# Kernel optimization log

Hardware: AMD Instinct MI355X
Metric: run time of the kernel (lower is better)

Reference implementation:

```python
import jax, jax.numpy as jnp
import numpy as np

EPS = 1e-6
NEG = 0.2  # leaky-relu negative slope
OBJ_C = 6

def _knn(x, k):
    # x: [B,3,N] -> [B,N,k] indices of k nearest neighbors (incl. self)
    xx = jnp.sum(x * x, axis=1)
    inner = jnp.einsum('bdn,bdm->bnm', x, x)
    pd = 2.0 * inner - xx[:, :, None] - xx[:, None, :]  # negative sq dist
    return jax.lax.top_k(pd, k)[1]

def _gather_pts(xt, idx):
    # xt [B,N,D], idx [B,N,k] -> [B,N,k,D]
    return xt[jnp.arange(xt.shape[0])[:, None, None], idx]

def _vn_lin(W, x):
    # channel-mixing linear over VN channel dim: x [B,Cin,3,...]
    return jnp.einsum('oc,bc...->bo...', W, x)

def _vn_bn(x, g, b, eps=1e-5):
    # VNBatchNorm with batch statistics on vector norms
    n = jnp.linalg.norm(x, axis=2) + EPS          # [B,C,*spatial]
    axes = (0,) + tuple(range(2, n.ndim))
    m = jnp.mean(n, axes, keepdims=True)
    v = jnp.var(n, axes, keepdims=True)
    shp = (1, -1) + (1,) * (n.ndim - 2)
    nb = g.reshape(shp) * (n - m) / jnp.sqrt(v + eps) + b.reshape(shp)
    return x / n[:, :, None] * nb[:, :, None]

def _vn_leaky(p, d):
    dot = jnp.sum(p * d, axis=2, keepdims=True)
    dsq = jnp.sum(d * d, axis=2, keepdims=True)
    return NEG * p + (1.0 - NEG) * jnp.where(dot >= 0, p, p - (dot / (dsq + EPS)) * d)

def _vn_block(x, wf, wd, g=None, b=None):
    # VNLinearLeakyReLU
    p = _vn_lin(wf, x)
    if g is not None:
        p = _vn_bn(p, g, b)
    return _vn_leaky(p, _vn_lin(wd, x))

def _surface_feature(coord, k):
    # coord [B,3,N] -> [B,3(chan),3(vec),N,k]: (nb-ctr, ctr, nb x ctr)
    idx = _knn(coord, k)
    xt = coord.transpose(0, 2, 1)                                  # [B,N,3]
    nb = _gather_pts(xt, idx)[:, :, :, None, :]                    # [B,N,k,1,3]
    ctr = jnp.broadcast_to(xt[:, :, None, None, :], nb.shape)
    f = jnp.concatenate([nb - ctr, ctr, jnp.cross(nb, ctr, axis=-1)], axis=3)
    return f.transpose(0, 3, 4, 1, 2)

def _neighbor_feature(x, coord, k):
    # x [B,C,3,N], knn over coord -> [B,C,3,N,k]
    B, C, _, N = x.shape
    idx = _knn(coord, k)
    xt = x.reshape(B, C * 3, N).transpose(0, 2, 1)                 # [B,N,C*3]
    f = _gather_pts(xt, idx).reshape(B, N, k, C, 3)
    return f.transpose(0, 3, 4, 1, 2)

def _vn_maxpool_down(x, coord, wd, rate):
    # x [B,C,3,N,k]: stride-subsample points, VN-max over k neighbors
    x = x[:, :, :, ::rate, :]
    coord_d = coord[:, :, ::rate]
    dot = jnp.sum(x * _vn_lin(wd, x), axis=2)                      # [B,C,Nd,k]
    idx = jnp.argmax(dot, axis=-1)
    xm = jnp.take_along_axis(x, idx[:, :, None, :, None], axis=-1)[..., 0]
    return xm, coord_d

def _nearest_index(t, s):
    # t [B,N,3], s [B,M,3] -> argmin sq-dist index [B,N]
    d = jnp.sum(t * t, -1)[:, :, None] - 2.0 * jnp.einsum('bnd,bmd->bnm', t, s) + jnp.sum(s * s, -1)[:, None, :]
    return jnp.argmin(d, axis=-1)

def _index_points(x, idx):
    # x [B,C,3,M], idx [B,N] -> [B,C,3,N]
    xt = x.transpose(0, 3, 1, 2)
    return xt[jnp.arange(x.shape[0])[:, None], idx].transpose(0, 2, 3, 1)

def _conv_bn_relu(x, w, b, g, be, eps=1e-5):
    # 1x1 Conv1d + BatchNorm1d (batch stats) + ReLU
    y = jnp.einsum('oc,bcn->bon', w, x) + b[None, :, None]
    m = jnp.mean(y, (0, 2), keepdims=True)
    v = jnp.var(y, (0, 2), keepdims=True)
    return jax.nn.relu(g[None, :, None] * (y - m) / jnp.sqrt(v + eps) + be[None, :, None])

def _forward(x, norm, cat_id, wf0, wd0, g0, b0, wf1, wd1, g1, b1, wp1, wf2, wd2, g2, b2, wf3, wd3, g3, b3, wp2, wf4, wd4, g4, b4, wv1f, wv1d, wv2f, wv2d, w3, ws1, cb1, sg1, sb1, ws2, cb2, sg2, sb2, ws3, cb3, sg3, sb3):
    B, _, _, N = x.shape
    coord = x.reshape(B, 3, N)
    one_hot = jax.nn.one_hot(cat_id, OBJ_C, dtype=x.dtype)
    x0 = _vn_block(_surface_feature(coord, 20), wf0, wd0, g0, b0).mean(-1)   # [B,42,3,N]
    x1 = _vn_block(x0, wf1, wd1, g1, b1)
    x2, coord2 = _vn_maxpool_down(_neighbor_feature(x1, coord, 4), coord, wp1, 4)
    x2 = _vn_block(x2, wf2, wd2, g2, b2)                                     # [B,84,3,N/4]
    x3 = _vn_block(x2, wf3, wd3, g3, b3)
    x4, coord4 = _vn_maxpool_down(_neighbor_feature(x3, coord2, 4), coord2, wp2, 4)
    x4 = _vn_block(x4, wf4, wd4, g4, b4)                                     # [B,168,3,N/16]
    ct = coord.transpose(0, 2, 1)
    i1 = _nearest_index(ct, coord2.transpose(0, 2, 1))
    i2 = _nearest_index(ct, coord4.transpose(0, 2, 1))
    eqv = jnp.concatenate([x0, x1, _index_points(x2, i1), _index_points(x3, i1), _index_points(x4, i2)], axis=1)  # [B,420,3,N]
    mean_feat = eqv.mean(-1, keepdims=True)                                  # [B,420,3,1]
    z = _vn_block(mean_feat, wv1f, wv1d)
    z = _vn_block(z, wv2f, wv2d)
    z = jnp.einsum('bcvm,kc->bvkm', z, w3)                                   # [B,3,2,1]
    inv_gl = jnp.einsum('bijm,bjkm->bikm', mean_feat, z).reshape(B, -1, 1)   # [B,840,1]
    inv_0 = jnp.broadcast_to(inv_gl, (B, inv_gl.shape[1], N))
    inv_1 = jnp.sum(mean_feat * coord[:, None], axis=2)                      # [B,420,N]
    oh = jnp.broadcast_to(one_hot[:, :, None], (B, OBJ_C, N))
    inv = jnp.concatenate([norm, inv_0, inv_1, oh], axis=1)                  # [B,1267,N]
    inv = _conv_bn_relu(inv, ws1, cb1, sg1, sb1)
    inv = _conv_bn_relu(inv, ws2, cb2, sg2, sb2)
    inv = _conv_bn_relu(inv, ws3, cb3, sg3, sb3)                             # [B,420,N]
    return eqv, mean_feat, inv, inv_gl

def setup_inputs():
    key = jax.random.key(0)
    ki = iter(jax.random.split(key, 40))
    B, N, D = 4, 2048, 42
    def lin(o, c):
        return jax.random.normal(next(ki), (o, c), jnp.float32) / float(np.sqrt(c))
    inp = dict(
        x=jax.random.normal(next(ki), (B, 1, 3, N), jnp.float32),
        norm=jax.random.normal(next(ki), (B, 1, N), jnp.float32),
        cat_id=jax.random.randint(next(ki), (B,), 0, OBJ_C),
        wf0=lin(D, 3), wd0=lin(D, 3), g0=jnp.ones(D), b0=jnp.zeros(D),
        wf1=lin(D, D), wd1=lin(D, D), g1=jnp.ones(D), b1=jnp.zeros(D),
        wp1=lin(D, D),
        wf2=lin(2 * D, D), wd2=lin(2 * D, D), g2=jnp.ones(2 * D), b2=jnp.zeros(2 * D),
        wf3=lin(2 * D, 2 * D), wd3=lin(2 * D, 2 * D), g3=jnp.ones(2 * D), b3=jnp.zeros(2 * D),
        wp2=lin(2 * D, 2 * D),
        wf4=lin(4 * D, 2 * D), wd4=lin(4 * D, 2 * D), g4=jnp.ones(4 * D), b4=jnp.zeros(4 * D),
        wv1f=lin(5 * D, 10 * D), wv1d=lin(5 * D, 10 * D),
        wv2f=lin(2 * D, 5 * D), wv2d=lin(2 * D, 5 * D),
        w3=lin(2, 2 * D),
        ws1=lin(1024, 1267), cb1=jnp.zeros(1024), sg1=jnp.ones(1024), sb1=jnp.zeros(1024),
        ws2=lin(512, 1024), cb2=jnp.zeros(512), sg2=jnp.ones(512), sb2=jnp.zeros(512),
        ws3=lin(420, 512), cb3=jnp.zeros(420), sg3=jnp.ones(420), sb3=jnp.zeros(420),
    )
    return inp

def reference(x, norm, cat_id, wf0, wd0, g0, b0, wf1, wd1, g1, b1, wp1, wf2, wd2, g2, b2, wf3, wd3, g3, b3, wp2, wf4, wd4, g4, b4, wv1f, wv1d, wv2f, wv2d, w3, ws1, cb1, sg1, sb1, ws2, cb2, sg2, sb2, ws3, cb3, sg3, sb3):
    return _forward(x, norm, cat_id, wf0, wd0, g0, b0, wf1, wd1, g1, b1, wp1, wf2, wd2, g2, b2, wf3, wd3, g3, b3, wp2, wf4, wd4, g4, b4, wv1f, wv1d, wv2f, wv2d, w3, ws1, cb1, sg1, sb1, ws2, cb2, sg2, sb2, ws3, cb3, sg3, sb3)
```

## Files before the change

kernel.cpp:

```cpp
#include <hip/hip_runtime.h>
#include <hip/hip_bf16.h>
#include <cstdint>
#include <cstddef>

#define NTOT 2048
#define BTOT 4

typedef short bf16x8 __attribute__((ext_vector_type(8)));
typedef float f32x4 __attribute__((ext_vector_type(4)));

__device__ inline unsigned short f2b(float v) {
    __hip_bfloat16 h = __float2bfloat16(v);
    return *reinterpret_cast<unsigned short*>(&h);
}

static const size_t WS_IDX20 = 0;
static const size_t WS_X1T   = 163840;
static const size_t WS_X0    = 1638400;
static const size_t WS_X1    = 3702784;
static const size_t WS_XM2   = 5767168;
static const size_t WS_X2    = 6025216;
static const size_t WS_X3    = 6541312;
static const size_t WS_IDX42 = 7057408;
static const size_t WS_XM4   = 7059456;
static const size_t WS_X4    = 7188480;
static const size_t WS_I1    = 7446528;
static const size_t WS_I2    = 7454720;
static const size_t WS_MF    = 7462912;
static const size_t WS_INVGL = 7467952;
static const size_t WS_STATS = 7471312;
static const size_t WS_CST   = 7472992;
static const size_t WS_CB    = 7480320;
static const size_t WS_AB    = 7484416;
static const size_t WS_W0    = 7496704;
static const size_t WS_Z1    = 7497728;
static const size_t WS_Z2    = 7500288;
static const size_t WS_X3T   = 7501312;
static const size_t WS_W2B   = 13378560;
static const size_t WS_W3B   = 13640704;
static const size_t WS_Y1B   = 0;
static const size_t WS_Y2T   = 7480320;
static const size_t WS_Y2B   = 4194304;
static const size_t WS_Y3T   = 13771776;

#define ZERO_SPAN_BYTES ((7476904 - 7462912) * 4)

#define ST0_OFF 0
#define ST1_OFF 84
#define ST2_OFF 168
#define ST3_OFF 336
#define ST4_OFF 504
#define CST1_OFF 0
#define CST2_OFF 2048
#define CST3_OFF 3072

#define OUT_EQV   0
#define OUT_MF    10321920
#define OUT_INV   10326960
#define OUT_INVGL 13767600

template <int SLOTS, int K, int NQ>
__global__ __launch_bounds__(256)
void knn_reg_kernel(const float* __restrict__ coord, int cand_stride, int q_stride,
                    int* __restrict__ out_idx, int q_cnt)
{
#pragma clang fp contract(off)
    constexpr int Q = SLOTS / 8;
    int b = blockIdx.y;
    int wave = threadIdx.x >> 6, lane = threadIdx.x & 63;
// ... 170 lines not shown
            float cx = ctr[ps * 3], cy = ctr[ps * 3 + 1], cz = ctr[ps * 3 + 2];
            const float* nb = &nbc[ps * 60];
            float sf = 0.f, sf2 = 0.f;
            for (int k = 0; k < 20; ++k) {
                float nx = nb[k * 3], ny = nb[k * 3 + 1], nz = nb[k * 3 + 2];
                float dx = nx - cx, dy = ny - cy, dz = nz - cz;
                float crx = ny * cz - nz * cy;
                float cry = nz * cx - nx * cz;
                float crz = nx * cy - ny * cx;
                float p0 = w0 * dx + w1 * cx + w2 * crx;
                float p1 = w0 * dy + w1 * cy + w2 * cry;
                float p2 = w0 * dz + w1 * cz + w2 * crz;
                float nrm = sqrtf(p0 * p0 + p1 * p1 + p2 * p2) + 1e-6f;
                sf += nrm; sf2 += nrm * nrm;
            }
            s += (double)sf; s2 += (double)sf2;
        }
    }
    if (active) { red[0][ps][o] = s; red[1][ps][o] = s2; }
    __syncthreads();
    if (t < 42) {
        double a = 0.0, a2 = 0.0;
#pragma unroll
        for (int p = 0; p < 6; ++p) { a += red[0][p][t]; a2 += red[1][p][t]; }
        atomicAdd(&stats[t], a);
        atomicAdd(&stats[42 + t], a2);
    }
}

__global__ __launch_bounds__(256)
void apply0_kernel(const float* __restrict__ coord, const int* __restrict__ idx20,
                   const float* __restrict__ wf0, const float* __restrict__ wd0,
                   const float* __restrict__ g0, const float* __restrict__ b0,
                   const double* __restrict__ stats, float* __restrict__ x0)
{
    __shared__ float nbc[360];
    __shared__ float ctr[18];
    int t = threadIdx.x;
    int b = blockIdx.y;
    int ps = t / 42, o = t - ps * 42;
    int n0 = blockIdx.x * 6;
    if (t < 120) {
        int pl = t / 20, k = t - pl * 20;
        int n = n0 + pl; if (n > NTOT - 1) n = NTOT - 1;
        int m = idx20[((size_t)(b * NTOT + n)) * 20 + k];
        nbc[t * 3 + 0] = coord[(b * 3 + 0) * NTOT + m];
        nbc[t * 3 + 1] = coord[(b * 3 + 1) * NTOT + m];
        nbc[t * 3 + 2] = coord[(b * 3 + 2) * NTOT + m];
    }
    if (t >= 128 && t < 146) {
        int i = t - 128; int pl = i / 3, vd = i - pl * 3;
        int n = n0 + pl; if (n > NTOT - 1) n = NTOT - 1;
        ctr[i] = coord[(b * 3 + vd) * NTOT + n];
    }
    __syncthreads();
    int n = n0 + ps;
    if (ps >= 6 || n >= NTOT) return;
    double S1 = stats[o], S2 = stats[42 + o];
    double md = S1 / 163840.0;
    float m = (float)md;
    float var = (float)(S2 / 163840.0 - md * md);
    float gs = g0[o] / sqrtf(var + 1e-5f);
    float bb = b0[o];
    float wa0 = wf0[o * 3], wa1 = wf0[o * 3 + 1], wa2 = wf0[o * 3 + 2];
    float wb0 = wd0[o * 3], wb1 = wd0[o * 3 + 1], wb2 = wd0[o * 3 + 2];
    float cx = ctr[ps * 3], cy = ctr[ps * 3 + 1], cz = ctr[ps * 3 + 2];
    const float* nb = &nbc[ps * 60];
    float a0 = 0.f, a1 = 0.f, a2 = 0.f;
    for (int k = 0; k < 20; ++k) {
        float nx = nb[k * 3], ny = nb[k * 3 + 1], nz = nb[k * 3 + 2];
        float dx = nx - cx, dy = ny - cy, dz = nz - cz;
        float crx = ny * cz - nz * cy;
        float cry = nz * cx - nx * cz;
        float crz = nx * cy - ny * cx;
        float p0 = wa0 * dx + wa1 * cx + wa2 * crx;
        float p1 = wa0 * dy + wa1 * cy + wa2 * cry;
        float p2 = wa0 * dz + wa1 * cz + wa2 * crz;
        float d0 = wb0 * dx + wb1 * cx + wb2 * crx;
        float d1 = wb0 * dy + wb1 * cy + wb2 * cry;
        float d2 = wb0 * dz + wb1 * cz + wb2 * crz;
        float nrm = sqrtf(p0 * p0 + p1 * p1 + p2 * p2) + 1e-6f;
        float nbv = gs * (nrm - m) + bb;
        float sc = nbv / nrm;
        p0 *= sc; p1 *= sc; p2 *= sc;
        float dot = p0 * d0 + p1 * d1 + p2 * d2;
        float dsq = d0 * d0 + d1 * d1 + d2 * d2 + 1e-6f;
        float tq = fminf(dot, 0.f) / dsq;
        a0 += 0.2f * p0 + 0.8f * (p0 - tq * d0);
        a1 += 0.2f * p1 + 0.8f * (p1 - tq * d1);
        a2 += 0.2f * p2 + 0.8f * (p2 - tq * d2);
    }
    x0[((size_t)(b * 42 + o) * 3 + 0) * NTOT + n] = a0 / 20.0f;
    x0[((size_t)(b * 42 + o) * 3 + 1) * NTOT + n] = a1 / 20.0f;
    x0[((size_t)(b * 42 + o) * 3 + 2) * NTOT + n] = a2 / 20.0f;
}

template <int Ci, int Co, int PTS, int NT, int NIT>
__global__ __launch_bounds__(NT)
void vn_stats_kernel(const float* __restrict__ xin,
                     const float* __restrict__ wf,
                     double* __restrict__ stats, int Npts)
{
    constexpr int Ci3 = Ci * 3;
    constexpr int STRIDE = Ci3 + 1;
    __shared__ float col[PTS * STRIDE];
    __shared__ double red[2][PTS][Co];
    int t = threadIdx.x;
    int b = blockIdx.y;
    int ps = t / Co;
    int o = t - ps * Co;
    bool active = ps < PTS;
    double s = 0.0, s2 = 0.0;
    int base = blockIdx.x * (PTS * NIT);
    for (int it = 0; it < NIT; ++it) {
        int pt0 = base + it * PTS;
        __syncthreads();
        for (int i = t; i < PTS * Ci3; i += NT) {
            int pl = i / Ci3, off = i - pl * Ci3;
            int pt = pt0 + pl; if (pt >= Npts) pt = Npts - 1;
            col[pl * STRIDE + off] = xin[(size_t)(b * 3 * Ci + off) * Npts + pt];
        }
        __syncthreads();
        if (active && pt0 + ps < Npts) {
            const float* cl = &col[ps * STRIDE];
            const float* wr = wf + o * Ci;
            float p0 = 0.f, p1 = 0.f, p2 = 0.f;
#pragma unroll
            for (int c = 0; c < Ci; ++c) {
                float w = wr[c];
                p0 += w * cl[3 * c]; p1 += w * cl[3 * c + 1]; p2 += w * cl[3 * c + 2];
            }
            float nrm = sqrtf(p0 * p0 + p1 * p1 + p2 * p2) + 1e-6f;
            s += (double)nrm; s2 += (double)nrm * (double)nrm;
        }
    }
    if (active) { red[0][ps][o] = s; red[1][ps][o] = s2; }
    __syncthreads();
    if (t < Co) {
        double a = 0.0, a2 = 0.0;
#pragma unroll
        for (int p = 0; p < PTS; ++p) { a += red[0][p][t]; a2 += red[1][p][t]; }
        atomicAdd(&stats[t], a);
        atomicAdd(&stats[Co + t], a2);
    }
}

template <int Ci, int Co, int PTS, int NT, bool WT>
__global__ __launch_bounds__(NT)
void vn_apply_kernel(const float* __restrict__ xin,
                     const float* __restrict__ wf,
                     const float* __restrict__ wd,
                     const float* __restrict__ g,
                     const float* __restrict__ bbp,
                     const double* __restrict__ stats,
                     double count, int Npts,
                     float* __restrict__ xout,
                     float* __restrict__ xt)
{
    constexpr int Ci3 = Ci * 3;
    constexpr int STRIDE = Ci3 + 1;
    constexpr int CH = Co * 3;
    __shared__ float col[PTS * STRIDE];
    int t = threadIdx.x;
    int b = blockIdx.y;
    int ps = t / Co;
    int o = t - ps * Co;
    bool active = ps < PTS;
    float m = 0.f, gs = 0.f, bb = 0.f;
    if (active) {
        double S1 = stats[o], S2 = stats[Co + o];
        double md = S1 / count;
        m = (float)md;
        float var = (float)(S2 / count - md * md);
        gs = g[o] / sqrtf(var + 1e-5f);
        bb = bbp[o];
    }
    int pt0 = blockIdx.x * PTS;
    for (int i = t; i < PTS * Ci3; i += NT) {
        int pl = i / Ci3, off = i - pl * Ci3;
        int pt = pt0 + pl; if (pt >= Npts) pt = Npts - 1;
        col[pl * STRIDE + off] = xin[(size_t)(b * 3 * Ci + off) * Npts + pt];
    }
    __syncthreads();
    int pt = pt0 + ps;
    if (!active || pt >= Npts) return;
    const float* cl = &col[ps * STRIDE];
    const float* wr = wf + o * Ci;
    const float* wdr = wd + o * Ci;
    float p0 = 0.f, p1 = 0.f, p2 = 0.f, d0 = 0.f, d1 = 0.f, d2 = 0.f;
#pragma unroll
    for (int c = 0; c < Ci; ++c) {
        float c0 = cl[3 * c], c1 = cl[3 * c + 1], c2 = cl[3 * c + 2];
        float w = wr[c];
        p0 += w * c0; p1 += w * c1; p2 += w * c2;
        float w2 = wdr[c];
        d0 += w2 * c0; d1 += w2 * c1; d2 += w2 * c2;
    }
    float nrm = sqrtf(p0 * p0 + p1 * p1 + p2 * p2) + 1e-6f;
    float nb = gs * (nrm - m) + bb;
    float sc = nb / nrm;
    p0 *= sc; p1 *= sc; p2 *= sc;
    float dot = p0 * d0 + p1 * d1 + p2 * d2;
    float dsq = d0 * d0 + d1 * d1 + d2 * d2 + 1e-6f;
    float tq = fminf(dot, 0.f) / dsq;
    float r0 = p0 - tq * d0, r1 = p1 - tq * d1, r2 = p2 - tq * d2;
    float o0 = 0.2f * p0 + 0.8f * r0;
    float o1 = 0.2f * p1 + 0.8f * r1;
    float o2 = 0.2f * p2 + 0.8f * r2;
    xout[((size_t)(b * Co + o) * 3 + 0) * Npts + pt] = o0;
    xout[((size_t)(b * Co + o) * 3 + 1) * Npts + pt] = o1;
    xout[((size_t)(b * Co + o) * 3 + 2) * Npts + pt] = o2;
    if (WT) {
        float* tp = xt + ((size_t)(b * Npts + pt)) * CH + o * 3;
        tp[0] = o0; tp[1] = o1; tp[2] = o2;
    }
}

__global__ void vn_pool_kernel(const float* __restrict__ xint,
                               const int* __restrict__ idx, long long sb, int sq,
                               const float* __restrict__ wp,
                               float* __restrict__ xout,
                               int C, int Np, int Nq)
{
#pragma clang fp contract(off)
    __shared__ float nb[4 * 84 * 3];
    int b = blockIdx.y;
    int q = blockIdx.x;
    const int* ir = idx + b * sb + (long long)q * sq;
    int CH = C * 3;
    for (int kk = 0; kk < 4; ++kk) {
        int mm = ir[kk];
        const float* src = xint + ((size_t)(b * Np + mm)) * CH;
        for (int t = threadIdx.x; t < CH; t += blockDim.x)
            nb[kk * CH + t] = src[t];
    }
    __syncthreads();
    int o = threadIdx.x;
    if (o >= C) return;
    const float* wr = wp + o * C;
    float best = -3.4e38f;
    int bk = 0;
    for (int kk = 0; kk < 4; ++kk) {
        const float* cl = &nb[kk * CH];
        float d0 = 0.f, d1 = 0.f, d2 = 0.f;
        for (int c = 0; c < C; ++c) {
            float w = wr[c];
            d0 += w * cl[3 * c]; d1 += w * cl[3 * c + 1]; d2 += w * cl[3 * c + 2];
// ... 12 lines not shown
                           const float* __restrict__ x4,
                           const int* __restrict__ i1, const int* __restrict__ i2,
                           float* __restrict__ out_eqv, float* __restrict__ mfw)
{
    __shared__ float wsum[4];
    int n = blockIdx.x * 256 + threadIdx.x;
    int cv = blockIdx.y;
    int b = blockIdx.z;
    int cc = cv / 3, v = cv % 3;
    float val;
    if (cc < 42)
        val = x0[((size_t)(b * 42 + cc) * 3 + v) * NTOT + n];
    else if (cc < 84)
        val = x1[((size_t)(b * 42 + (cc - 42)) * 3 + v) * NTOT + n];
    else if (cc < 168) {
        int m = i1[b * NTOT + n];
        val = x2[((size_t)(b * 84 + (cc - 84)) * 3 + v) * 512 + m];
    } else if (cc < 252) {
        int m = i1[b * NTOT + n];
        val = x3[((size_t)(b * 84 + (cc - 168)) * 3 + v) * 512 + m];
    } else {
        int m = i2[b * NTOT + n];
        val = x4[((size_t)(b * 168 + (cc - 252)) * 3 + v) * 128 + m];
    }
    out_eqv[((size_t)(b * 1260 + cv)) * NTOT + n] = val;
    float s = val;
    for (int off = 32; off; off >>= 1) s += __shfl_down(s, off);
    if ((threadIdx.x & 63) == 0) wsum[threadIdx.x >> 6] = s;
    __syncthreads();
    if (threadIdx.x == 0)
        atomicAdd(&mfw[b * 1260 + cv], (wsum[0] + wsum[1]) + (wsum[2] + wsum[3]));
}

__global__ void mf_finalize_kernel(float* __restrict__ mfw, float* __restrict__ out_mf)
{
    int i = blockIdx.x * 256 + threadIdx.x;
    if (i < 5040) {
        float m = mfw[i] / 2048.0f;
        mfw[i] = m;
        out_mf[i] = m;
    }
}

__global__ __launch_bounds__(256)
void z1_kernel(const float* __restrict__ mfw,
               const float* __restrict__ wv1f, const float* __restrict__ wv1d,
               float* __restrict__ z1ws)
{
    __shared__ float mf[1260];
    int b = blockIdx.y;
    int wave = threadIdx.x >> 6, lane = threadIdx.x & 63;
    for (int i = threadIdx.x; i < 1260; i += 256) mf[i] = mfw[b * 1260 + i];
    __syncthreads();
    int o = blockIdx.x * 4 + wave;
    if (o >= 210) return;
    const float* wr  = wv1f + (size_t)o * 420;
    const float* wdr = wv1d + (size_t)o * 420;
    float p0 = 0.f, p1 = 0.f, p2 = 0.f, d0 = 0.f, d1 = 0.f, d2 = 0.f;
    for (int c = lane; c < 420; c += 64) {
        float m0 = mf[3 * c], m1 = mf[3 * c + 1], m2 = mf[3 * c + 2];
        float w = wr[c];
        p0 += w * m0; p1 += w * m1; p2 += w * m2;
        float w2 = wdr[c];
        d0 += w2 * m0; d1 += w2 * m1; d2 += w2 * m2;
    }
    for (int off = 32; off; off >>= 1) {
        p0 += __shfl_down(p0, off); p1 += __shfl_down(p1, off);
        p2 += __shfl_down(p2, off); d0 += __shfl_down(d0, off);
        d1 += __shfl_down(d1, off); d2 += __shfl_down(d2, off);
    }
    if (lane == 0) {
        float dot = p0 * d0 + p1 * d1 + p2 * d2;
        float r0, r1, r2;
        if (dot >= 0.f) { r0 = p0; r1 = p1; r2 = p2; }
        else {
            float tq = dot / (d0 * d0 + d1 * d1 + d2 * d2 + 1e-6f);
            r0 = p0 - tq * d0; r1 = p1 - tq * d1; r2 = p2 - tq * d2;
        }
        z1ws[b * 630 + o * 3]     = 0.2f * p0 + 0.8f * r0;
        z1ws[b * 630 + o * 3 + 1] = 0.2f * p1 + 0.8f * r1;
        z1ws[b * 630 + o * 3 + 2] = 0.2f * p2 + 0.8f * r2;
    }
}

__global__ __launch_bounds__(256)
void z2_kernel(const float* __restrict__ z1ws,
               const float* __restrict__ wv2f, const float* __restrict__ wv2d,
               float* __restrict__ z2ws)
{
    __shared__ float zl[630];
    int b = blockIdx.y;
    int wave = threadIdx.x >> 6, lane = threadIdx.x & 63;
    for (int i = threadIdx.x; i < 630; i += 256) zl[i] = z1ws[b * 630 + i];
    __syncthreads();
    int o = blockIdx.x * 4 + wave;
    if (o >= 84) return;
    const float* wr  = wv2f + (size_t)o * 210;
    const float* wdr = wv2d + (size_t)o * 210;
    float p0 = 0.f, p1 = 0.f, p2 = 0.f, d0 = 0.f, d1 = 0.f, d2 = 0.f;
    for (int c = lane; c < 210; c += 64) {
        float m0 = zl[3 * c], m1 = zl[3 * c + 1], m2 = zl[3 * c + 2];
        float w = wr[c];
        p0 += w * m0; p1 += w * m1; p2 += w * m2;
        float w2 = wdr[c];
        d0 += w2 * m0; d1 += w2 * m1; d2 += w2 * m2;
    }
    for (int off = 32; off; off >>= 1) {
        p0 += __shfl_down(p0, off); p1 += __shfl_down(p1, off);
        p2 += __shfl_down(p2, off); d0 += __shfl_down(d0, off);
        d1 += __shfl_down(d1, off); d2 += __shfl_down(d2, off);
    }
    if (lane == 0) {
        float dot = p0 * d0 + p1 * d1 + p2 * d2;
        float r0, r1, r2;
        if (dot >= 0.f) { r0 = p0; r1 = p1; r2 = p2; }
        else {
            float tq = dot / (d0 * d0 + d1 * d1 + d2 * d2 + 1e-6f);
            r0 = p0 - tq * d0; r1 = p1 - tq * d1; r2 = p2 - tq * d2;
        }
        z2ws[b * 252 + o * 3]     = 0.2f * p0 + 0.8f * r0;
        z2ws[b * 252 + o * 3 + 1] = 0.2f * p1 + 0.8f * r1;
        z2ws[b * 252 + o * 3 + 2] = 0.2f * p2 + 0.8f * r2;
    }
}

__global__ void z3invgl_kernel(const float* __restrict__ mfw,
                               const float* __restrict__ z2ws,
                               const float* __restrict__ w3,
                               float* __restrict__ invgl_ws,
                               float* __restrict__ out_invgl)
{
    __shared__ float z2[252];
    __shared__ float z3[6];
    __shared__ float mf[1260];
    int b = blockIdx.x;
    int t = threadIdx.x;
    for (int i = t; i < 252; i += 256) z2[i] = z2ws[b * 252 + i];
    for (int i = t; i < 1260; i += 256) mf[i] = mfw[b * 1260 + i];
    __syncthreads();
    if (t < 6) {
        int v = t / 2, kt = t % 2;
        float s = 0.f;
        for (int c = 0; c < 84; ++c) s += z2[c * 3 + v] * w3[kt * 84 + c];
        z3[v * 2 + kt] = s;
    }
    __syncthreads();
    for (int i = t; i < 840; i += 256) {
        int ii = i / 2, kt = i % 2;
        float s = mf[ii * 3] * z3[0 + kt] + mf[ii * 3 + 1] * z3[2 + kt] +
                  mf[ii * 3 + 2] * z3[4 + kt];
        invgl_ws[b * 840 + i] = s;
        out_invgl[b * 840 + i] = s;
    }
}

__global__ __launch_bounds__(256)
void conv1_coef_kernel(const float* __restrict__ ws1,
                       const float* __restrict__ invgl,
                       const float* __restrict__ mfw,
                       const int* __restrict__ cat,
                       float* __restrict__ cb, float* __restrict__ ab,
                       float* __restrict__ w0)
{
    int wave = threadIdx.x >> 6, lane = threadIdx.x & 63;
    int o = blockIdx.x * 4 + wave;
    int b = blockIdx.y;
    const float* wr = ws1 + (size_t)o * 1267;
    float s = 0.f;
    for (int j = lane; j < 840; j += 64)
        s += wr[1 + j] * invgl[b * 840 + j];
    float a0 = 0.f, a1 = 0.f, a2 = 0.f;
    for (int i = lane; i < 420; i += 64) {
        float w = wr[841 + i];
        a0 += w * mfw[b * 1260 + i * 3];
        a1 += w * mfw[b * 1260 + i * 3 + 1];
        a2 += w * mfw[b * 1260 + i * 3 + 2];
    }
    for (int off = 32; off; off >>= 1) {
        s  += __shfl_down(s, off);
        a0 += __shfl_down(a0, off);
        a1 += __shfl_down(a1, off);
        a2 += __shfl_down(a2, off);
    }
// ... 248 lines not shown
    const float* w3   = (const float*)d_in[29];
    const float* ws1  = (const float*)d_in[30];
    const float* sg1  = (const float*)d_in[32];
    const float* sb1  = (const float*)d_in[33];
    const float* ws2  = (const float*)d_in[34];
    const float* sg2  = (const float*)d_in[36];
    const float* sb2  = (const float*)d_in[37];
    const float* ws3  = (const float*)d_in[38];
    const float* sg3  = (const float*)d_in[40];
    const float* sb3  = (const float*)d_in[41];

    float* ws = (float*)d_ws;
    float* out = (float*)d_out;

    int*    idx20 = (int*)(ws + WS_IDX20);
    float*  x1t   = ws + WS_X1T;
    float*  x0    = ws + WS_X0;
    float*  x1    = ws + WS_X1;
    float*  xm2   = ws + WS_XM2;
    float*  x2    = ws + WS_X2;
    float*  x3    = ws + WS_X3;
    int*    idx42 = (int*)(ws + WS_IDX42);
    float*  xm4   = ws + WS_XM4;
    float*  x4    = ws + WS_X4;
    int*    i1p   = (int*)(ws + WS_I1);
    int*    i2p   = (int*)(ws + WS_I2);
    float*  mfw   = ws + WS_MF;
    float*  invgl = ws + WS_INVGL;
    double* st    = (double*)(ws + WS_STATS);
    float*  cst   = ws + WS_CST;
    float*  cb    = ws + WS_CB;
    float*  ab    = ws + WS_AB;
    float*  w0    = ws + WS_W0;
    float*  z1ws  = ws + WS_Z1;
    float*  z2ws  = ws + WS_Z2;
    float*  x3t   = ws + WS_X3T;
    unsigned short* w2b  = (unsigned short*)(ws + WS_W2B);
    unsigned short* w3b  = (unsigned short*)(ws + WS_W3B);
    unsigned short* y1b  = (unsigned short*)(ws + WS_Y1B);
    float*  y2t   = ws + WS_Y2T;
    unsigned short* y2b  = (unsigned short*)(ws + WS_Y2B);
    float*  y3t   = ws + WS_Y3T;

    hipMemsetAsync((void*)mfw, 0, ZERO_SPAN_BYTES, stream);

    wconv_kernel<<<dim3(4, 512), 256, 0, stream>>>(ws2, w2b, 512, 1024, 1024);
    wconv_kernel<<<dim3(2, 512), 256, 0, stream>>>(ws3, w3b, 420, 512, 512);

    knn_reg_kernel<32, 20, 2><<<dim3(256, 4), 256, 0, stream>>>(xc, 1, 1, idx20, 2048);

    stats0_kernel<<<dim3(43, 4), 256, 0, stream>>>(xc, idx20, wf0, st + ST0_OFF);
    apply0_kernel<<<dim3(342, 4), 256, 0, stream>>>(xc, idx20, wf0, wd0, g0, b0,
                                                    st + ST0_OFF, x0);

    vn_stats_kernel<42, 42, 6, 256, 8><<<dim3(43, 4), 256, 0, stream>>>(
        x0, wf1, st + ST1_OFF, 2048);
    vn_apply_kernel<42, 42, 6, 256, true><<<dim3(342, 4), 256, 0, stream>>>(
        x0, wf1, wd1, g1, b1, st + ST1_OFF, 8192.0, 2048, x1, x1t);

    vn_pool_kernel<<<dim3(512, 4), 256, 0, stream>>>(x1t, idx20, 40960LL, 80, wp1, xm2,
                                                     42, 2048, 512);
    vn_stats_kernel<42, 84, 3, 256, 8><<<dim3(22, 4), 256, 0, stream>>>(
        xm2, wf2, st + ST2_OFF, 512);
    vn_apply_kernel<42, 84, 3, 256, false><<<dim3(171, 4), 256, 0, stream>>>(
        xm2, wf2, wd2, g2, b2, st + ST2_OFF, 2048.0, 512, x2, nullptr);
    vn_stats_kernel<84, 84, 3, 256, 8><<<dim3(22, 4), 256, 0, stream>>>(
        x2, wf3, st + ST3_OFF, 512);
    vn_apply_kernel<84, 84, 3, 256, true><<<dim3(171, 4), 256, 0, stream>>>(
        x2, wf3, wd3, g3, b3, st + ST3_OFF, 2048.0, 512, x3, x3t);

    knn_reg_kernel<8, 4, 1><<<dim3(32, 4), 256, 0, stream>>>(xc, 4, 16, idx42, 128);
    vn_pool_kernel<<<dim3(128, 4), 256, 0, stream>>>(x3t, idx42, 512LL, 4, wp2, xm4,
                                                     84, 512, 128);
    vn_stats_kernel<84, 168, 3, 512, 4><<<dim3(11, 4), 512, 0, stream>>>(
        xm4, wf4, st + ST4_OFF, 128);
    vn_apply_kernel<84, 168, 3, 512, false><<<dim3(43, 4), 512, 0, stream>>>(
        xm4, wf4, wd4, g4, b4, st + ST4_OFF, 512.0, 128, x4, nullptr);

    nearest_dual_kernel<<<dim3(512, 4), 256, 0, stream>>>(xc, i1p, i2p);

    eqv_kernel<<<dim3(8, 1260, 4), 256, 0, stream>>>(x0, x1, x2, x3, x4, i1p, i2p,
                                                     out + OUT_EQV, mfw);
    mf_finalize_kernel<<<20, 256, 0, stream>>>(mfw, out + OUT_MF);

    z1_kernel<<<dim3(53, 4), 256, 0, stream>>>(mfw, wv1f, wv1d, z1ws);
    z2_kernel<<<dim3(21, 4), 256, 0, stream>>>(z1ws, wv2f, wv2d, z2ws);
    z3invgl_kernel<<<4, 256, 0, stream>>>(mfw, z2ws, w3, invgl, out + OUT_INVGL);

    conv1_coef_kernel<<<dim3(256, 4), 256, 0, stream>>>(ws1, invgl, mfw, cat, cb, ab, w0);
    y1_stats_kernel<<<dim3(4, 32), 256, 0, stream>>>(cb, ab, w0, xc, normv,
                                                     cst + CST1_OFF);
    y1_bnrelu_kernel<<<dim3(4, 32), 256, 0, stream>>>(cb, ab, w0, xc, normv,
                                                      cst + CST1_OFF, sg1, sb1, y1b);

    gemm_mfma_kernel<<<dim3(128, 8), 256, 0, stream>>>(y1b, w2b, y2t, cst + CST2_OFF,
                                                       1024, 512);
    bnreluT_kernel<<<16384, 256, 0, stream>>>(y2t, cst + CST2_OFF, sg2, sb2, y2b,
                                              512, 511);

    gemm_mfma_kernel<<<dim3(128, 7), 256, 0, stream>>>(y2b, w3b, y3t, cst + CST3_OFF,
                                                       512, 420);
    bnrelu_outT_kernel<<<dim3(128, 7), 256, 0, stream>>>(y3t, cst + CST3_OFF, sg3, sb3,
                                                         out + OUT_INV);
}
```

Baseline: 585.8 us.

## Fuse next-layer BN stats into apply kernels and merge z-head kernels

apply0 and the layer-2 vn_apply now compute the next layer's batch-norm norm statistics from their freshly produced outputs held in shared memory. This removes the separate vn_stats passes over x0 and x2. Each block loops over several point groups to amortize the atomics, which cuts the grid to 43 and 22 blocks per batch. The mf finalize, z1, z2 and z3 head kernels are merged into one 4-block kernel, which saves launches but serializes the head matvecs on far fewer threads.

```diff
diff --git a/kernel.cpp b/kernel.cpp
--- a/kernel.cpp
+++ b/kernel.cpp
@@ -33,8 +33,6 @@
 static const size_t WS_CB    = 7480320;
 static const size_t WS_AB    = 7484416;
 static const size_t WS_W0    = 7496704;
-static const size_t WS_Z1    = 7497728;
-static const size_t WS_Z2    = 7500288;
 static const size_t WS_X3T   = 7501312;
 static const size_t WS_W2B   = 13378560;
 static const size_t WS_W3B   = 13640704;
@@ -271,67 +269,108 @@
 void apply0_kernel(const float* __restrict__ coord, const int* __restrict__ idx20,
                    const float* __restrict__ wf0, const float* __restrict__ wd0,
                    const float* __restrict__ g0, const float* __restrict__ b0,
-                   const double* __restrict__ stats, float* __restrict__ x0)
+                   const double* __restrict__ stats,
+                   const float* __restrict__ wf1, double* __restrict__ stats1,
+                   float* __restrict__ x0)
 {
     __shared__ float nbc[360];
     __shared__ float ctr[18];
+    __shared__ float colout[6][127];
+    __shared__ double red[2][6][42];
     int t = threadIdx.x;
     int b = blockIdx.y;
     int ps = t / 42, o = t - ps * 42;
-    int n0 = blockIdx.x * 6;
-    if (t < 120) {
-        int pl = t / 20, k = t - pl * 20;
-        int n = n0 + pl; if (n > NTOT - 1) n = NTOT - 1;
-        int m = idx20[((size_t)(b * NTOT + n)) * 20 + k];
-        nbc[t * 3 + 0] = coord[(b * 3 + 0) * NTOT + m];
-        nbc[t * 3 + 1] = coord[(b * 3 + 1) * NTOT + m];
-        nbc[t * 3 + 2] = coord[(b * 3 + 2) * NTOT + m];
-    }
-    if (t >= 128 && t < 146) {
-        int i = t - 128; int pl = i / 3, vd = i - pl * 3;
-        int n = n0 + pl; if (n > NTOT - 1) n = NTOT - 1;
-        ctr[i] = coord[(b * 3 + vd) * NTOT + n];
-    }
-    __syncthreads();
-    int n = n0 + ps;
-    if (ps >= 6 || n >= NTOT) return;
-    double S1 = stats[o], S2 = stats[42 + o];
-    double md = S1 / 163840.0;
-    float m = (float)md;
-    float var = (float)(S2 / 163840.0 - md * md);
-    float gs = g0[o] / sqrtf(var + 1e-5f);
-    float bb = b0[o];
-    float wa0 = wf0[o * 3], wa1 = wf0[o * 3 + 1], wa2 = wf0[o * 3 + 2];
-    float wb0 = wd0[o * 3], wb1 = wd0[o * 3 + 1], wb2 = wd0[o * 3 + 2];
-    float cx = ctr[ps * 3], cy = ctr[ps * 3 + 1], cz = ctr[ps * 3 + 2];
-    const float* nb = &nbc[ps * 60];
-    float a0 = 0.f, a1 = 0.f, a2 = 0.f;
-    for (int k = 0; k < 20; ++k) {
-        float nx = nb[k * 3], ny = nb[k * 3 + 1], nz = nb[k * 3 + 2];
-        float dx = nx - cx, dy = ny - cy, dz = nz - cz;
-        float crx = ny * cz - nz * cy;
-        float cry = nz * cx - nx * cz;
-        float crz = nx * cy - ny * cx;
-        float p0 = wa0 * dx + wa1 * cx + wa2 * crx;
-        float p1 = wa0 * dy + wa1 * cy + wa2 * cry;
-        float p2 = wa0 * dz + wa1 * cz + wa2 * crz;
-        float d0 = wb0 * dx + wb1 * cx + wb2 * crx;
-        float d1 = wb0 * dy + wb1 * cy + wb2 * cry;
-        float d2 = wb0 * dz + wb1 * cz + wb2 * crz;
-        float nrm = sqrtf(p0 * p0 + p1 * p1 + p2 * p2) + 1e-6f;
-        float nbv = gs * (nrm - m) + bb;
-        float sc = nbv / nrm;
-        p0 *= sc; p1 *= sc; p2 *= sc;
-        float dot = p0 * d0 + p1 * d1 + p2 * d2;
-        float dsq = d0 * d0 + d1 * d1 + d2 * d2 + 1e-6f;
-        float tq = fminf(dot, 0.f) / dsq;
-        a0 += 0.2f * p0 + 0.8f * (p0 - tq * d0);
-        a1 += 0.2f * p1 + 0.8f * (p1 - tq * d1);
-        a2 += 0.2f * p2 + 0.8f * (p2 - tq * d2);
-    }
-    x0[((size_t)(b * 42 + o) * 3 + 0) * NTOT + n] = a0 / 20.0f;
-    x0[((size_t)(b * 42 + o) * 3 + 1) * NTOT + n] = a1 / 20.0f;
-    x0[((size_t)(b * 42 + o) * 3 + 2) * NTOT + n] = a2 / 20.0f;
+    bool active = ps < 6;
+    float m = 0.f, gs = 0.f, bb = 0.f;
+    float wa0 = 0.f, wa1 = 0.f, wa2 = 0.f, wb0 = 0.f, wb1 = 0.f, wb2 = 0.f;
+    if (active) {
+        double S1 = stats[o], S2 = stats[42 + o];
+        double md = S1 / 163840.0;
+        m = (float)md;
+        float var = (float)(S2 / 163840.0 - md * md);
+        gs = g0[o] / sqrtf(var + 1e-5f);
+        bb = b0[o];
+        wa0 = wf0[o * 3]; wa1 = wf0[o * 3 + 1]; wa2 = wf0[o * 3 + 2];
+        wb0 = wd0[o * 3]; wb1 = wd0[o * 3 + 1]; wb2 = wd0[o * 3 + 2];
+    }
+    double s1 = 0.0, s2 = 0.0;
+    int base = blockIdx.x * 48;
+    for (int it = 0; it < 8; ++it) {
+        int n0 = base + it * 6;
+        __syncthreads();
+        if (t < 120) {
+            int pl = t / 20, k = t - pl * 20;
+            int n = n0 + pl; if (n > NTOT - 1) n = NTOT - 1;
+            int mm = idx20[((size_t)(b * NTOT + n)) * 20 + k];
+            nbc[t * 3 + 0] = coord[(b * 3 + 0) * NTOT + mm];
+            nbc[t * 3 + 1] = coord[(b * 3 + 1) * NTOT + mm];
+            nbc[t * 3 + 2] = coord[(b * 3 + 2) * NTOT + mm];
+        }
+        if (t >= 128 && t < 146) {
+            int i = t - 128; int pl = i / 3, vd = i - pl * 3;
+            int n = n0 + pl; if (n > NTOT - 1) n = NTOT - 1;
+            ctr[i] = coord[(b * 3 + vd) * NTOT + n];
+        }
+        __syncthreads();
+        int n = n0 + ps;
+        bool valid = active && n < NTOT;
+        if (valid) {
+            float cx = ctr[ps * 3], cy = ctr[ps * 3 + 1], cz = ctr[ps * 3 + 2];
+            const float* nb = &nbc[ps * 60];
+            float a0 = 0.f, a1 = 0.f, a2 = 0.f;
+            for (int k = 0; k < 20; ++k) {
+                float nx = nb[k * 3], ny = nb[k * 3 + 1], nz = nb[k * 3 + 2];
+                float dx = nx - cx, dy = ny - cy, dz = nz - cz;
+                float crx = ny * cz - nz * cy;
+                float cry = nz * cx - nx * cz;
+                float crz = nx * cy - ny * cx;
+                float p0 = wa0 * dx + wa1 * cx + wa2 * crx;
+                float p1 = wa0 * dy + wa1 * cy + wa2 * cry;
+                float p2 = wa0 * dz + wa1 * cz + wa2 * crz;
+                float d0 = wb0 * dx + wb1 * cx + wb2 * crx;
+                float d1 = wb0 * dy + wb1 * cy + wb2 * cry;
+                float d2 = wb0 * dz + wb1 * cz + wb2 * crz;
+                float nrm = sqrtf(p0 * p0 + p1 * p1 + p2 * p2) + 1e-6f;
+                float nbv = gs * (nrm - m) + bb;
+                float sc = nbv / nrm;
+                p0 *= sc; p1 *= sc; p2 *= sc;
+                float dot = p0 * d0 + p1 * d1 + p2 * d2;
+                float dsq = d0 * d0 + d1 * d1 + d2 * d2 + 1e-6f;
+                float tq = fminf(dot, 0.f) / dsq;
+                a0 += 0.2f * p0 + 0.8f * (p0 - tq * d0);
+                a1 += 0.2f * p1 + 0.8f * (p1 - tq * d1);
+                a2 += 0.2f * p2 + 0.8f * (p2 - tq * d2);
+            }
+            float o0 = a0 / 20.0f, o1 = a1 / 20.0f, o2 = a2 / 20.0f;
+            x0[((size_t)(b * 42 + o) * 3 + 0) * NTOT + n] = o0;
+            x0[((size_t)(b * 42 + o) * 3 + 1) * NTOT + n] = o1;
+            x0[((size_t)(b * 42 + o) * 3 + 2) * NTOT + n] = o2;
+            colout[ps][o * 3 + 0] = o0;
+            colout[ps][o * 3 + 1] = o1;
+            colout[ps][o * 3 + 2] = o2;
+        }
+        __syncthreads();
+        if (valid) {
+            const float* wr = wf1 + o * 42;
+            const float* cl = colout[ps];
+            float p0 = 0.f, p1 = 0.f, p2 = 0.f;
+            for (int c = 0; c < 42; ++c) {
+                float w = wr[c];
+                p0 += w * cl[3 * c]; p1 += w * cl[3 * c + 1]; p2 += w * cl[3 * c + 2];
+            }
+            float nrm = sqrtf(p0 * p0 + p1 * p1 + p2 * p2) + 1e-6f;
+            s1 += (double)nrm; s2 += (double)(nrm * nrm);
+        }
+    }
+    if (active) { red[0][ps][o] = s1; red[1][ps][o] = s2; }
+    __syncthreads();
+    if (t < 42) {
+        double a = 0.0, a2 = 0.0;
+#pragma unroll
+        for (int p = 0; p < 6; ++p) { a += red[0][p][t]; a2 += red[1][p][t]; }
+        atomicAdd(&stats1[t], a);
+        atomicAdd(&stats1[42 + t], a2);
+    }
 }
 
 template <int Ci, int Co, int PTS, int NT, int NIT>
@@ -384,7 +423,7 @@
     }
 }
 
-template <int Ci, int Co, int PTS, int NT, bool WT>
+template <int Ci, int Co, int PTS, int NT, int NIT, bool WT, int CoN>
 __global__ __launch_bounds__(NT)
 void vn_apply_kernel(const float* __restrict__ xin,
                      const float* __restrict__ wf,
@@ -394,12 +433,16 @@
                      const double* __restrict__ stats,
                      double count, int Npts,
                      float* __restrict__ xout,
-                     float* __restrict__ xt)
+                     float* __restrict__ xt,
+                     const float* __restrict__ wfn,
+                     double* __restrict__ statsn)
 {
     constexpr int Ci3 = Ci * 3;
     constexpr int STRIDE = Ci3 + 1;
     constexpr int CH = Co * 3;
     __shared__ float col[PTS * STRIDE];
+    __shared__ float colout[(CoN > 0) ? PTS * (CH + 1) : 1];
+    __shared__ double redn[(CoN > 0) ? 2 * PTS * CoN : 1];
     int t = threadIdx.x;
     int b = blockIdx.y;
     int ps = t / Co;
@@ -414,44 +457,87 @@
         gs = g[o] / sqrtf(var + 1e-5f);
         bb = bbp[o];
     }
-    int pt0 = blockIdx.x * PTS;
-    for (int i = t; i < PTS * Ci3; i += NT) {
-        int pl = i / Ci3, off = i - pl * Ci3;
-        int pt = pt0 + pl; if (pt >= Npts) pt = Npts - 1;
-        col[pl * STRIDE + off] = xin[(size_t)(b * 3 * Ci + off) * Npts + pt];
-    }
-    __syncthreads();
-    int pt = pt0 + ps;
-    if (!active || pt >= Npts) return;
-    const float* cl = &col[ps * STRIDE];
-    const float* wr = wf + o * Ci;
-    const float* wdr = wd + o * Ci;
-    float p0 = 0.f, p1 = 0.f, p2 = 0.f, d0 = 0.f, d1 = 0.f, d2 = 0.f;
-#pragma unroll
-    for (int c = 0; c < Ci; ++c) {
-        float c0 = cl[3 * c], c1 = cl[3 * c + 1], c2 = cl[3 * c + 2];
-        float w = wr[c];
-        p0 += w * c0; p1 += w * c1; p2 += w * c2;
-        float w2 = wdr[c];
-        d0 += w2 * c0; d1 += w2 * c1; d2 += w2 * c2;
-    }
-    float nrm = sqrtf(p0 * p0 + p1 * p1 + p2 * p2) + 1e-6f;
-    float nb = gs * (nrm - m) + bb;
-    float sc = nb / nrm;
-    p0 *= sc; p1 *= sc; p2 *= sc;
-    float dot = p0 * d0 + p1 * d1 + p2 * d2;
-    float dsq = d0 * d0 + d1 * d1 + d2 * d2 + 1e-6f;
-    float tq = fminf(dot, 0.f) / dsq;
-    float r0 = p0 - tq * d0, r1 = p1 - tq * d1, r2 = p2 - tq * d2;
-    float o0 = 0.2f * p0 + 0.8f * r0;
-    float o1 = 0.2f * p1 + 0.8f * r1;
-    float o2 = 0.2f * p2 + 0.8f * r2;
-    xout[((size_t)(b * Co + o) * 3 + 0) * Npts + pt] = o0;
-    xout[((size_t)(b * Co + o) * 3 + 1) * Npts + pt] = o1;
-    xout[((size_t)(b * Co + o) * 3 + 2) * Npts + pt] = o2;
-    if (WT) {
-        float* tp = xt + ((size_t)(b * Npts + pt)) * CH + o * 3;
-        tp[0] = o0; tp[1] = o1; tp[2] = o2;
+    double sn1 = 0.0, sn2 = 0.0;
+    for (int itn = 0; itn < NIT; ++itn) {
+        int pt0 = (blockIdx.x * NIT + itn) * PTS;
+        __syncthreads();
+        for (int i = t; i < PTS * Ci3; i += NT) {
+            int pl = i / Ci3, off = i - pl * Ci3;
+            int pt = pt0 + pl; if (pt >= Npts) pt = Npts - 1;
+            col[pl * STRIDE + off] = xin[(size_t)(b * 3 * Ci + off) * Npts + pt];
+        }
+        __syncthreads();
+        int pt = pt0 + ps;
+        bool valid = active && pt < Npts;
+        if (valid) {
+            const float* cl = &col[ps * STRIDE];
+            const float* wr = wf + o * Ci;
+            const float* wdr = wd + o * Ci;
+            float p0 = 0.f, p1 = 0.f, p2 = 0.f, d0 = 0.f, d1 = 0.f, d2 = 0.f;
+#pragma unroll
+            for (int c = 0; c < Ci; ++c) {
+                float c0 = cl[3 * c], c1 = cl[3 * c + 1], c2 = cl[3 * c + 2];
+                float w = wr[c];
+                p0 += w * c0; p1 += w * c1; p2 += w * c2;
+                float w2 = wdr[c];
+                d0 += w2 * c0; d1 += w2 * c1; d2 += w2 * c2;
+            }
+            float nrm = sqrtf(p0 * p0 + p1 * p1 + p2 * p2) + 1e-6f;
+            float nb = gs * (nrm - m) + bb;
+            float sc = nb / nrm;
+            p0 *= sc; p1 *= sc; p2 *= sc;
+            float dot = p0 * d0 + p1 * d1 + p2 * d2;
+            float dsq = d0 * d0 + d1 * d1 + d2 * d2 + 1e-6f;
+            float tq = fminf(dot, 0.f) / dsq;
+            float r0 = p0 - tq * d0, r1 = p1 - tq * d1, r2 = p2 - tq * d2;
+            float o0 = 0.2f * p0 + 0.8f * r0;
+            float o1 = 0.2f * p1 + 0.8f * r1;
+            float o2 = 0.2f * p2 + 0.8f * r2;
+            xout[((size_t)(b * Co + o) * 3 + 0) * Npts + pt] = o0;
+            xout[((size_t)(b * Co + o) * 3 + 1) * Npts + pt] = o1;
+            xout[((size_t)(b * Co + o) * 3 + 2) * Npts + pt] = o2;
+            if (WT) {
+                float* tp = xt + ((size_t)(b * Npts + pt)) * CH + o * 3;
+                tp[0] = o0; tp[1] = o1; tp[2] = o2;
+            }
+            if constexpr (CoN > 0) {
+                colout[ps * (CH + 1) + o * 3 + 0] = o0;
+                colout[ps * (CH + 1) + o * 3 + 1] = o1;
+                colout[ps * (CH + 1) + o * 3 + 2] = o2;
+            }
+        }
+        if constexpr (CoN > 0) {
+            __syncthreads();
+            if (valid) {
+                const float* wrn = wfn + o * Co;
+                const float* cl2 = &colout[ps * (CH + 1)];
+                float p0 = 0.f, p1 = 0.f, p2 = 0.f;
+#pragma unroll
+                for (int c = 0; c < Co; ++c) {
+                    float w = wrn[c];
+                    p0 += w * cl2[3 * c]; p1 += w * cl2[3 * c + 1]; p2 += w * cl2[3 * c + 2];
+                }
+                float nrm = sqrtf(p0 * p0 + p1 * p1 + p2 * p2) + 1e-6f;
+                sn1 += (double)nrm; sn2 += (double)(nrm * nrm);
+            }
+        }
+    }
+    if constexpr (CoN > 0) {
+        if (active) {
+            redn[(0 * PTS + ps) * CoN + o] = sn1;
+            redn[(1 * PTS + ps) * CoN + o] = sn2;
+        }
+        __syncthreads();
+        if (t < CoN) {
+            double a = 0.0, a2 = 0.0;
+#pragma unroll
+            for (int p = 0; p < PTS; ++p) {
+                a  += redn[(0 * PTS + p) * CoN + t];
+                a2 += redn[(1 * PTS + p) * CoN + t];
+            }
+            atomicAdd(&statsn[t], a);
+            atomicAdd(&statsn[CoN + t], a2);
+        }
     }
 }
 
@@ -530,123 +616,75 @@
         atomicAdd(&mfw[b * 1260 + cv], (wsum[0] + wsum[1]) + (wsum[2] + wsum[3]));
 }
 
-__global__ void mf_finalize_kernel(float* __restrict__ mfw, float* __restrict__ out_mf)
-{
-    int i = blockIdx.x * 256 + threadIdx.x;
-    if (i < 5040) {
-        float m = mfw[i] / 2048.0f;
-        mfw[i] = m;
-        out_mf[i] = m;
-    }
-}
-
 __global__ __launch_bounds__(256)
-void z1_kernel(const float* __restrict__ mfw,
-               const float* __restrict__ wv1f, const float* __restrict__ wv1d,
-               float* __restrict__ z1ws)
+void zhead_kernel(float* __restrict__ mfw, float* __restrict__ out_mf,
+                  const float* __restrict__ wv1f, const float* __restrict__ wv1d,
+                  const float* __restrict__ wv2f, const float* __restrict__ wv2d,
+                  const float* __restrict__ w3,
+                  float* __restrict__ invgl_ws, float* __restrict__ out_invgl)
 {
     __shared__ float mf[1260];
-    int b = blockIdx.y;
-    int wave = threadIdx.x >> 6, lane = threadIdx.x & 63;
-    for (int i = threadIdx.x; i < 1260; i += 256) mf[i] = mfw[b * 1260 + i];
-    __syncthreads();
-    int o = blockIdx.x * 4 + wave;
-    if (o >= 210) return;
-    const float* wr  = wv1f + (size_t)o * 420;
-    const float* wdr = wv1d + (size_t)o * 420;
-    float p0 = 0.f, p1 = 0.f, p2 = 0.f, d0 = 0.f, d1 = 0.f, d2 = 0.f;
-    for (int c = lane; c < 420; c += 64) {
-        float m0 = mf[3 * c], m1 = mf[3 * c + 1], m2 = mf[3 * c + 2];
-        float w = wr[c];
-        p0 += w * m0; p1 += w * m1; p2 += w * m2;
-        float w2 = wdr[c];
-        d0 += w2 * m0; d1 += w2 * m1; d2 += w2 * m2;
-    }
-    for (int off = 32; off; off >>= 1) {
-        p0 += __shfl_down(p0, off); p1 += __shfl_down(p1, off);
-        p2 += __shfl_down(p2, off); d0 += __shfl_down(d0, off);
-        d1 += __shfl_down(d1, off); d2 += __shfl_down(d2, off);
-    }
-    if (lane == 0) {
-        float dot = p0 * d0 + p1 * d1 + p2 * d2;
-        float r0, r1, r2;
-        if (dot >= 0.f) { r0 = p0; r1 = p1; r2 = p2; }
-        else {
-            float tq = dot / (d0 * d0 + d1 * d1 + d2 * d2 + 1e-6f);
-            r0 = p0 - tq * d0; r1 = p1 - tq * d1; r2 = p2 - tq * d2;
-        }
-        z1ws[b * 630 + o * 3]     = 0.2f * p0 + 0.8f * r0;
-        z1ws[b * 630 + o * 3 + 1] = 0.2f * p1 + 0.8f * r1;
-        z1ws[b * 630 + o * 3 + 2] = 0.2f * p2 + 0.8f * r2;
-    }
-}
-
-__global__ __launch_bounds__(256)
-void z2_kernel(const float* __restrict__ z1ws,
-               const float* __restrict__ wv2f, const float* __restrict__ wv2d,
-               float* __restrict__ z2ws)
-{
-    __shared__ float zl[630];
-    int b = blockIdx.y;
-    int wave = threadIdx.x >> 6, lane = threadIdx.x & 63;
-    for (int i = threadIdx.x; i < 630; i += 256) zl[i] = z1ws[b * 630 + i];
-    __syncthreads();
-    int o = blockIdx.x * 4 + wave;
-    if (o >= 84) return;
-    const float* wr  = wv2f + (size_t)o * 210;
-    const float* wdr = wv2d + (size_t)o * 210;
-    float p0 = 0.f, p1 = 0.f, p2 = 0.f, d0 = 0.f, d1 = 0.f, d2 = 0.f;
-    for (int c = lane; c < 210; c += 64) {
-        float m0 = zl[3 * c], m1 = zl[3 * c + 1], m2 = zl[3 * c + 2];
-        float w = wr[c];
-        p0 += w * m0; p1 += w * m1; p2 += w * m2;
-        float w2 = wdr[c];
-        d0 += w2 * m0; d1 += w2 * m1; d2 += w2 * m2;
-    }
-    for (int off = 32; off; off >>= 1) {
-        p0 += __shfl_down(p0, off); p1 += __shfl_down(p1, off);
-        p2 += __shfl_down(p2, off); d0 += __shfl_down(d0, off);
-        d1 += __shfl_down(d1, off); d2 += __shfl_down(d2, off);
-    }
-    if (lane == 0) {
-        float dot = p0 * d0 + p1 * d1 + p2 * d2;
-        float r0, r1, r2;
-        if (dot >= 0.f) { r0 = p0; r1 = p1; r2 = p2; }
-        else {
-            float tq = dot / (d0 * d0 + d1 * d1 + d2 * d2 + 1e-6f);
-            r0 = p0 - tq * d0; r1 = p1 - tq * d1; r2 = p2 - tq * d2;
-        }
-        z2ws[b * 252 + o * 3]     = 0.2f * p0 + 0.8f * r0;
-        z2ws[b * 252 + o * 3 + 1] = 0.2f * p1 + 0.8f * r1;
-        z2ws[b * 252 + o * 3 + 2] = 0.2f * p2 + 0.8f * r2;
-    }
-}
-
-__global__ void z3invgl_kernel(const float* __restrict__ mfw,
-                               const float* __restrict__ z2ws,
-                               const float* __restrict__ w3,
-                               float* __restrict__ invgl_ws,
-                               float* __restrict__ out_invgl)
-{
-    __shared__ float z2[252];
-    __shared__ float z3[6];
-    __shared__ float mf[1260];
+    __shared__ float z1l[630];
+    __shared__ float z2l[252];
+    __shared__ float z3l[6];
     int b = blockIdx.x;
     int t = threadIdx.x;
-    for (int i = t; i < 252; i += 256) z2[i] = z2ws[b * 252 + i];
-    for (int i = t; i < 1260; i += 256) mf[i] = mfw[b * 1260 + i];
+    for (int i = t; i < 1260; i += 256) {
+        float m = mfw[b * 1260 + i] / 2048.0f;
+        mfw[b * 1260 + i] = m;
+        out_mf[b * 1260 + i] = m;
+        mf[i] = m;
+    }
+    __syncthreads();
+    if (t < 210) {
+        const float* wr  = wv1f + (size_t)t * 420;
+        const float* wdr = wv1d + (size_t)t * 420;
+        float p0 = 0.f, p1 = 0.f, p2 = 0.f, d0 = 0.f, d1 = 0.f, d2 = 0.f;
+        for (int c = 0; c < 420; ++c) {
+            float m0 = mf[3 * c], m1 = mf[3 * c + 1], m2 = mf[3 * c + 2];
+            float w = wr[c];
+            p0 += w * m0; p1 += w * m1; p2 += w * m2;
+            float w2 = wdr[c];
+            d0 += w2 * m0; d1 += w2 * m1; d2 += w2 * m2;
+        }
+        float dot = p0 * d0 + p1 * d1 + p2 * d2;
+        float dsq = d0 * d0 + d1 * d1 + d2 * d2 + 1e-6f;
+        float tq = fminf(dot, 0.f) / dsq;
+        z1l[t * 3 + 0] = 0.2f * p0 + 0.8f * (p0 - tq * d0);
+        z1l[t * 3 + 1] = 0.2f * p1 + 0.8f * (p1 - tq * d1);
+        z1l[t * 3 + 2] = 0.2f * p2 + 0.8f * (p2 - tq * d2);
+    }
+    __syncthreads();
+    if (t < 84) {
+        const float* wr  = wv2f + (size_t)t * 210;
+        const float* wdr = wv2d + (size_t)t * 210;
+        float p0 = 0.f, p1 = 0.f, p2 = 0.f, d0 = 0.f, d1 = 0.f, d2 = 0.f;
+        for (int c = 0; c < 210; ++c) {
+            float m0 = z1l[3 * c], m1 = z1l[3 * c + 1], m2 = z1l[3 * c + 2];
+            float w = wr[c];
+            p0 += w * m0; p1 += w * m1; p2 += w * m2;
+            float w2 = wdr[c];
+            d0 += w2 * m0; d1 += w2 * m1; d2 += w2 * m2;
+        }
+        float dot = p0 * d0 + p1 * d1 + p2 * d2;
+        float dsq = d0 * d0 + d1 * d1 + d2 * d2 + 1e-6f;
+        float tq = fminf(dot, 0.f) / dsq;
+        z2l[t * 3 + 0] = 0.2f * p0 + 0.8f * (p0 - tq * d0);
+        z2l[t * 3 + 1] = 0.2f * p1 + 0.8f * (p1 - tq * d1);
+        z2l[t * 3 + 2] = 0.2f * p2 + 0.8f * (p2 - tq * d2);
+    }
     __syncthreads();
     if (t < 6) {
         int v = t / 2, kt = t % 2;
         float s = 0.f;
-        for (int c = 0; c < 84; ++c) s += z2[c * 3 + v] * w3[kt * 84 + c];
-        z3[v * 2 + kt] = s;
+        for (int c = 0; c < 84; ++c) s += z2l[c * 3 + v] * w3[kt * 84 + c];
+        z3l[v * 2 + kt] = s;
     }
     __syncthreads();
     for (int i = t; i < 840; i += 256) {
         int ii = i / 2, kt = i % 2;
-        float s = mf[ii * 3] * z3[0 + kt] + mf[ii * 3 + 1] * z3[2 + kt] +
-                  mf[ii * 3 + 2] * z3[4 + kt];
+        float s = mf[ii * 3] * z3l[0 + kt] + mf[ii * 3 + 1] * z3l[2 + kt] +
+                  mf[ii * 3 + 2] * z3l[4 + kt];
         invgl_ws[b * 840 + i] = s;
         out_invgl[b * 840 + i] = s;
     }
@@ -961,8 +999,6 @@
     float*  cb    = ws + WS_CB;
     float*  ab    = ws + WS_AB;
     float*  w0    = ws + WS_W0;
-    float*  z1ws  = ws + WS_Z1;
-    float*  z2ws  = ws + WS_Z2;
     float*  x3t   = ws + WS_X3T;
     unsigned short* w2b  = (unsigned short*)(ws + WS_W2B);
     unsigned short* w3b  = (unsigned short*)(ws + WS_W3B);
@@ -979,42 +1015,35 @@
     knn_reg_kernel<32, 20, 2><<<dim3(256, 4), 256, 0, stream>>>(xc, 1, 1, idx20, 2048);
 
     stats0_kernel<<<dim3(43, 4), 256, 0, stream>>>(xc, idx20, wf0, st + ST0_OFF);
-    apply0_kernel<<<dim3(342, 4), 256, 0, stream>>>(xc, idx20, wf0, wd0, g0, b0,
-                                                    st + ST0_OFF, x0);
-
-    vn_stats_kernel<42, 42, 6, 256, 8><<<dim3(43, 4), 256, 0, stream>>>(
-        x0, wf1, st + ST1_OFF, 2048);
-    vn_apply_kernel<42, 42, 6, 256, true><<<dim3(342, 4), 256, 0, stream>>>(
-        x0, wf1, wd1, g1, b1, st + ST1_OFF, 8192.0, 2048, x1, x1t);
+    apply0_kernel<<<dim3(43, 4), 256, 0, stream>>>(xc, idx20, wf0, wd0, g0, b0,
+                                                   st + ST0_OFF, wf1, st + ST1_OFF, x0);
+
+    vn_apply_kernel<42, 42, 6, 256, 1, true, 0><<<dim3(342, 4), 256, 0, stream>>>(
+        x0, wf1, wd1, g1, b1, st + ST1_OFF, 8192.0, 2048, x1, x1t, nullptr, nullptr);
 
     vn_pool_kernel<<<dim3(512, 4), 256, 0, stream>>>(x1t, idx20, 40960LL, 80, wp1, xm2,
                                                      42, 2048, 512);
     vn_stats_kernel<42, 84, 3, 256, 8><<<dim3(22, 4), 256, 0, stream>>>(
         xm2, wf2, st + ST2_OFF, 512);
-    vn_apply_kernel<42, 84, 3, 256, false><<<dim3(171, 4), 256, 0, stream>>>(
-        xm2, wf2, wd2, g2, b2, st + ST2_OFF, 2048.0, 512, x2, nullptr);
-    vn_stats_kernel<84, 84, 3, 256, 8><<<dim3(22, 4), 256, 0, stream>>>(
-        x2, wf3, st + ST3_OFF, 512);
-    vn_apply_kernel<84, 84, 3, 256, true><<<dim3(171, 4), 256, 0, stream>>>(
-        x2, wf3, wd3, g3, b3, st + ST3_OFF, 2048.0, 512, x3, x3t);
+    vn_apply_kernel<42, 84, 3, 256, 8, false, 84><<<dim3(22, 4), 256, 0, stream>>>(
+        xm2, wf2, wd2, g2, b2, st + ST2_OFF, 2048.0, 512, x2, nullptr, wf3, st + ST3_OFF);
+    vn_apply_kernel<84, 84, 3, 256, 1, true, 0><<<dim3(171, 4), 256, 0, stream>>>(
+        x2, wf3, wd3, g3, b3, st + ST3_OFF, 2048.0, 512, x3, x3t, nullptr, nullptr);
 
     knn_reg_kernel<8, 4, 1><<<dim3(32, 4), 256, 0, stream>>>(xc, 4, 16, idx42, 128);
     vn_pool_kernel<<<dim3(128, 4), 256, 0, stream>>>(x3t, idx42, 512LL, 4, wp2, xm4,
                                                      84, 512, 128);
     vn_stats_kernel<84, 168, 3, 512, 4><<<dim3(11, 4), 512, 0, stream>>>(
         xm4, wf4, st + ST4_OFF, 128);
-    vn_apply_kernel<84, 168, 3, 512, false><<<dim3(43, 4), 512, 0, stream>>>(
-        xm4, wf4, wd4, g4, b4, st + ST4_OFF, 512.0, 128, x4, nullptr);
+    vn_apply_kernel<84, 168, 3, 512, 1, false, 0><<<dim3(43, 4), 512, 0, stream>>>(
+        xm4, wf4, wd4, g4, b4, st + ST4_OFF, 512.0, 128, x4, nullptr, nullptr, nullptr);
 
     nearest_dual_kernel<<<dim3(512, 4), 256, 0, stream>>>(xc, i1p, i2p);
 
     eqv_kernel<<<dim3(8, 1260, 4), 256, 0, stream>>>(x0, x1, x2, x3, x4, i1p, i2p,
                                                      out + OUT_EQV, mfw);
-    mf_finalize_kernel<<<20, 256, 0, stream>>>(mfw, out + OUT_MF);
-
-    z1_kernel<<<dim3(53, 4), 256, 0, stream>>>(mfw, wv1f, wv1d, z1ws);
-    z2_kernel<<<dim3(21, 4), 256, 0, stream>>>(z1ws, wv2f, wv2d, z2ws);
-    z3invgl_kernel<<<4, 256, 0, stream>>>(mfw, z2ws, w3, invgl, out + OUT_INVGL);
+    zhead_kernel<<<4, 256, 0, stream>>>(mfw, out + OUT_MF, wv1f, wv1d, wv2f, wv2d,
+                                        w3, invgl, out + OUT_INVGL);
 
     conv1_coef_kernel<<<dim3(256, 4), 256, 0, stream>>>(ws1, invgl, mfw, cat, cb, ab, w0);
     y1_stats_kernel<<<dim3(4, 32), 256, 0, stream>>>(cb, ab, w0, xc, normv,
```

Measured after the change: 655.5 us. 1.12x slower.
